# Performance work log

Hardware: AMD Instinct MI355X
Metric: run time of the kernel (lower is better)

Reference implementation:

```python
import jax, jax.numpy as jnp
import numpy as np

D_MODEL = 512
D_FFN = 2048
N_LAYERS = 6
VOCAB = 1000
D_STATE = 16
D_CONV = 4
D_INNER = 2 * D_MODEL  # expand=2
DT_RANK = 32           # ceil(d_model/16)
B, LT, LS = 2, 512, 512


def _pos_encoding(length, d_model):
    pos = np.arange(length, dtype=np.float32)[:, None]
    div = np.exp(np.arange(0, d_model, 2, dtype=np.float32) * (-np.log(10000.0) / d_model))
    pe = np.zeros((length, d_model), np.float32)
    pe[:, 0::2] = np.sin(pos * div)
    pe[:, 1::2] = np.cos(pos * div)
    return jnp.asarray(pe)


def _layer_norm(x, g, b, eps=1e-6):
    m = x.mean(-1, keepdims=True)
    v = ((x - m) ** 2).mean(-1, keepdims=True)
    return (x - m) * jax.lax.rsqrt(v + eps) * g + b


def _mamba(x, in_w, conv_w, conv_b, xproj_w, dt_w, dt_b, A_log, Dskip, out_w):
    # x: (b, l, d_model)
    b, l, _ = x.shape
    xz = x @ in_w.T                                   # (b, l, 2*d_inner)
    xc, z = jnp.split(xz, 2, axis=-1)
    # causal depthwise conv over time
    xt = jnp.transpose(xc, (0, 2, 1))                 # (b, d_inner, l)
    xt = jnp.pad(xt, ((0, 0), (0, 0), (D_CONV - 1, 0)))
    xt = jax.lax.conv_general_dilated(
        xt, conv_w, window_strides=(1,), padding='VALID',
        feature_group_count=D_INNER, dimension_numbers=('NCH', 'OIH', 'NCH'))
    xc = jax.nn.silu(jnp.transpose(xt, (0, 2, 1)) + conv_b)  # (b, l, d_inner)
    dbl = xc @ xproj_w.T                              # (b, l, dt_rank + 2*n)
    dt, Bm, Cm = jnp.split(dbl, [DT_RANK, DT_RANK + D_STATE], axis=-1)
    dt = jax.nn.softplus(dt @ dt_w.T + dt_b)          # (b, l, d_inner)
    A = -jnp.exp(A_log)                               # (d_inner, n)

    def step(h, xs):
        dt_t, B_t, C_t, u_t = xs                      # (b,d),(b,n),(b,n),(b,d)
        dA = jnp.exp(dt_t[..., None] * A)             # (b, d, n)
        h = dA * h + (dt_t * u_t)[..., None] * B_t[:, None, :]
        y = jnp.einsum('bdn,bn->bd', h, C_t)
        return h, y

    h0 = jnp.zeros((b, D_INNER, D_STATE), x.dtype)
    xs = (jnp.swapaxes(dt, 0, 1), jnp.swapaxes(Bm, 0, 1),
          jnp.swapaxes(Cm, 0, 1), jnp.swapaxes(xc, 0, 1))
    _, ys = jax.lax.scan(step, h0, xs)                # ys: (l, b, d_inner)
    y = jnp.swapaxes(ys, 0, 1) + xc * Dskip
    y = y * jax.nn.silu(z)
    return y @ out_w.T                                # (b, l, d_model)


def setup_inputs() -> dict:
    key = jax.random.key(0)
    ks = iter(jax.random.split(key, 40))

    def rn(shape, s=0.02):
        return jax.random.normal(next(ks), shape, jnp.float32) * s

    def mamba_params():
        return dict(
            in_w=rn((N_LAYERS, 2 * D_INNER, D_MODEL)),
            conv_w=rn((N_LAYERS, D_INNER, 1, D_CONV), 0.1),
            conv_b=rn((N_LAYERS, D_INNER)),
            xproj=rn((N_LAYERS, DT_RANK + 2 * D_STATE, D_INNER)),
            dtw=rn((N_LAYERS, D_INNER, DT_RANK)),
            dtb=rn((N_LAYERS, D_INNER)),
            Alog=jnp.log(jnp.broadcast_to(jnp.arange(1.0, D_STATE + 1.0, dtype=jnp.float32), (N_LAYERS, D_INNER, D_STATE))),
            D=jnp.ones((N_LAYERS, D_INNER), jnp.float32),
            outw=rn((N_LAYERS, D_MODEL, D_INNER)),
        )

    ps, pc = mamba_params(), mamba_params()
    inp = {
        'src': jax.random.normal(next(ks), (B, LS, D_MODEL), jnp.float32),
        'tgt': jax.random.randint(next(ks), (B, LT), 0, VOCAB),
        'emb': rn((VOCAB, D_MODEL)),
        'in_w_s': ps['in_w'], 'conv_w_s': ps['conv_w'], 'conv_b_s': ps['conv_b'],
        'xproj_s': ps['xproj'], 'dtw_s': ps['dtw'], 'dtb_s': ps['dtb'],
        'Alog_s': ps['Alog'], 'D_s': ps['D'], 'outw_s': ps['outw'],
        'in_w_c': pc['in_w'], 'conv_w_c': pc['conv_w'], 'conv_b_c': pc['conv_b'],
        'xproj_c': pc['xproj'], 'dtw_c': pc['dtw'], 'dtb_c': pc['dtb'],
        'Alog_c': pc['Alog'], 'D_c': pc['D'], 'outw_c': pc['outw'],
        'ffn_w1': rn((N_LAYERS, D_FFN, D_MODEL)),
        'ffn_b1': jnp.zeros((N_LAYERS, D_FFN), jnp.float32),
        'ffn_w2': rn((N_LAYERS, D_MODEL, D_FFN)),
        'ffn_b2': jnp.zeros((N_LAYERS, D_MODEL), jnp.float32),
        'ln_g': jnp.ones((N_LAYERS, 3, D_MODEL), jnp.float32),
        'ln_b': jnp.zeros((N_LAYERS, 3, D_MODEL), jnp.float32),
        'fin_g': jnp.ones((D_MODEL,), jnp.float32),
        'fin_b': jnp.zeros((D_MODEL,), jnp.float32),
    }
    return inp


def reference(src, tgt, emb, in_w_s, conv_w_s, conv_b_s, xproj_s, dtw_s, dtb_s,
              Alog_s, D_s, outw_s, in_w_c, conv_w_c, conv_b_c, xproj_c, dtw_c,
              dtb_c, Alog_c, D_c, outw_c, ffn_w1, ffn_b1, ffn_w2, ffn_b2,
              ln_g, ln_b, fin_g, fin_b):
    # NormalizedEmbedding + sinusoidal positional encoding
    x = emb[tgt] * jnp.sqrt(jnp.asarray(D_MODEL, jnp.float32))
    x = x + _pos_encoding(LT, D_MODEL)[None]
    for i in range(N_LAYERS):
        # self mamba (post-norm, normalize_before=False)
        t2 = _mamba(x, in_w_s[i], conv_w_s[i], conv_b_s[i], xproj_s[i],
                    dtw_s[i], dtb_s[i], Alog_s[i], D_s[i], outw_s[i])
        x = _layer_norm(x + t2, ln_g[i, 0], ln_b[i, 0])
        # cross mamba over concat([memory, tgt]) then take last LT steps
        cat = jnp.concatenate([src, x], axis=1)
        t2 = _mamba(cat, in_w_c[i], conv_w_c[i], conv_b_c[i], xproj_c[i],
                    dtw_c[i], dtb_c[i], Alog_c[i], D_c[i], outw_c[i])[:, -LT:]
        x = _layer_norm(x + t2, ln_g[i, 1], ln_b[i, 1])
        # positionwise FFN
        h = jax.nn.relu(x @ ffn_w1[i].T + ffn_b1[i]) @ ffn_w2[i].T + ffn_b2[i]
        x = _layer_norm(x + h, ln_g[i, 2], ln_b[i, 2])
    return _layer_norm(x, fin_g, fin_b)
```

## Files before the change

kernel.cpp:

```cpp
#include <hip/hip_runtime.h>
#include <math.h>

#define DMODEL 512
#define DINNER 1024
#define DSTATE 16
#define DTRANK 32
#define NLAYERS 6
#define BB 2
#define LT 512
#define LS 512

typedef __attribute__((ext_vector_type(8))) short bf16x8;
typedef __attribute__((ext_vector_type(8))) unsigned short u16x8;
typedef __attribute__((ext_vector_type(4))) float f32x4;

__device__ __forceinline__ unsigned short f2bf(float f) {
  unsigned u = __float_as_uint(f);
  u += 0x7fffu + ((u >> 16) & 1u);
  return (unsigned short)(u >> 16);
}
__device__ __forceinline__ float bf2f(unsigned short u) {
  return __uint_as_float((unsigned)u << 16);
}

template<int EPI>
__device__ __forceinline__ float epi_apply(float acc, float b) {
  if (EPI == 1) { float v = acc + b; return v > 0.f ? v : 0.f; }
  if (EPI == 2) { return acc + b; }
  if (EPI == 3) { float v = acc + b; return fmaxf(v, 0.f) + log1pf(__expf(-fabsf(v))); }
  return acc;
}

__global__ __launch_bounds__(256) void cvt_all_kernel(
    const float* __restrict__ i0, const float* __restrict__ i1,
    const float* __restrict__ i2, const float* __restrict__ i3,
    const float* __restrict__ i4, const float* __restrict__ i5,
    const float* __restrict__ i6, const float* __restrict__ i7,
    const float* __restrict__ i8, const float* __restrict__ i9,
    unsigned short* __restrict__ outbase) {
  int i = blockIdx.x * 256 + threadIdx.x;
  if (i >= 8159232) return;
  const float* in; int off;
  if      (i < 1572864) { in = i0; off = i; }
  else if (i < 3145728) { in = i1; off = i - 1572864; }
  else if (i < 3244032) { in = i2; off = i - 3145728; }
  else if (i < 3342336) { in = i3; off = i - 3244032; }
  else if (i < 3391488) { in = i4; off = i - 3342336; }
  else if (i < 3440640) { in = i5; off = i - 3391488; }
  else if (i < 4227072) { in = i6; off = i - 3440640; }
  else if (i < 5013504) { in = i7; off = i - 4227072; }
  else if (i < 6586368) { in = i8; off = i - 5013504; }
  else                  { in = i9; off = i - 6586368; }
  float4 a = ((const float4*)in)[off];
  ushort4 o = make_ushort4(f2bf(a.x), f2bf(a.y), f2bf(a.z), f2bf(a.w));
  *(ushort4*)&outbase[(size_t)i * 4] = o;
}

__global__ __launch_bounds__(256) void embed_kernel(const int* __restrict__ tgt,
    const float* __restrict__ emb, float* __restrict__ X,
    unsigned short* __restrict__ Xb) {
  int i = blockIdx.x * 256 + threadIdx.x;
  int d = i & (DMODEL - 1);
  int bt = i >> 9;
  int t = bt & (LT - 1);
  int tok = tgt[bt];
  float div = __expf((float)(d & ~1) * (-9.210340371976184f / (float)DMODEL));
  float ang = (float)t * div;
  float pe = (d & 1) ? cosf(ang) : sinf(ang);
  float v = emb[(size_t)tok * DMODEL + d] * 22.627416997969522f + pe;
  X[i] = v;
  Xb[i] = f2bf(v);
}

__global__ __launch_bounds__(256) void catsrc_kernel(const float* __restrict__ src,
    unsigned short* __restrict__ CATb) {
  int i = blockIdx.x * 256 + threadIdx.x;
  int c8 = (i & 63) * 8;
  int r = i >> 6;
  int b = r >> 9, l = r & 511;
  const float* s = src + ((size_t)b * 512 + l) * DMODEL + c8;
  float4 a = *(const float4*)s;
  float4 bq = *(const float4*)(s + 4);
  u16x8 o;
  o[0] = f2bf(a.x); o[1] = f2bf(a.y); o[2] = f2bf(a.z); o[3] = f2bf(a.w);
  o[4] = f2bf(bq.x); o[5] = f2bf(bq.y); o[6] = f2bf(bq.z); o[7] = f2bf(bq.w);
  *(u16x8*)&CATb[((size_t)b * 1024 + l) * DMODEL + c8] = o;
}

template<int BK, int EPI, bool SPLIT, bool OUTB>
__global__ __launch_bounds__(256) void mgemmA(
    const unsigned short* __restrict__ A, const unsigned short* __restrict__ Bw,
    const float* __restrict__ bias, float* __restrict__ C,
    unsigned short* __restrict__ Cb, int M, int N, int K, int lda) {
  constexpr int PAD = BK + 8;
  constexpr int CHA = BK / 32;
  constexpr int CHB = BK / 16;
  __shared__ __align__(16) unsigned short As[64 * PAD];
  __shared__ __align__(16) unsigned short Bs[128 * PAD];
  const int tid = threadIdx.x;
  const int bn = blockIdx.x * 128;
  const int bm = blockIdx.y * 64;
  const int lane = tid & 63;
  const int w = tid >> 6;
  const int wr = (w >> 1) * 32;
  const int wc = (w & 1) * 64;
  const int l15 = lane & 15;
  const int l4 = lane >> 4;
  const int koff = l4 * 8;
  int kcnt = K, kbeg = 0;
  if (SPLIT) { kcnt = K / (int)gridDim.z; kbeg = blockIdx.z * kcnt; }
  const int nt = kcnt / BK;
  f32x4 acc[2][4] = {};

  int arow_[CHA], ak8_[CHA];
  const unsigned short* Ap[CHA];
#pragma unroll
  for (int i = 0; i < CHA; ++i) {
    int f = tid + 256 * i;
    arow_[i] = f / (BK / 8);
    ak8_[i] = (f % (BK / 8)) * 8;
    Ap[i] = A + (size_t)(bm + arow_[i]) * lda + kbeg + ak8_[i];
  }
  int brow_[CHB], bk8_[CHB];
  const unsigned short* Bp[CHB];
#pragma unroll
  for (int i = 0; i < CHB; ++i) {
    int f = tid + 256 * i;
    brow_[i] = f / (BK / 8);
    bk8_[i] = (f % (BK / 8)) * 8;
    Bp[i] = Bw + (size_t)(bn + brow_[i]) * K + kbeg + bk8_[i];
  }

  u16x8 av[CHA], bv[CHB];
#pragma unroll
  for (int i = 0; i < CHA; ++i) av[i] = *(const u16x8*)Ap[i];
#pragma unroll
  for (int i = 0; i < CHB; ++i) bv[i] = *(const u16x8*)Bp[i];

  for (int t = 0; t < nt; ++t) {
    __syncthreads();
#pragma unroll
    for (int i = 0; i < CHA; ++i) *(u16x8*)&As[arow_[i] * PAD + ak8_[i]] = av[i];
#pragma unroll
    for (int i = 0; i < CHB; ++i) *(u16x8*)&Bs[brow_[i] * PAD + bk8_[i]] = bv[i];
    if (t + 1 < nt) {
      int ko = (t + 1) * BK;
#pragma unroll
      for (int i = 0; i < CHA; ++i) av[i] = *(const u16x8*)(Ap[i] + ko);
#pragma unroll
      for (int i = 0; i < CHB; ++i) bv[i] = *(const u16x8*)(Bp[i] + ko);
    }
    __syncthreads();
#pragma unroll
    for (int kk = 0; kk < BK / 32; ++kk) {
      bf16x8 afr[2], bfr[4];
#pragma unroll
      for (int i = 0; i < 2; ++i)
        afr[i] = *(const bf16x8*)&As[(wr + i * 16 + l15) * PAD + kk * 32 + koff];
#pragma unroll
      for (int j = 0; j < 4; ++j)
        bfr[j] = *(const bf16x8*)&Bs[(wc + j * 16 + l15) * PAD + kk * 32 + koff];
#pragma unroll
      for (int fr = 0; fr < 2; ++fr)
#pragma unroll
        for (int fc = 0; fc < 4; ++fc)
          acc[fr][fc] = __builtin_amdgcn_mfma_f32_16x16x32_bf16(
              afr[fr], bfr[fc], acc[fr][fc], 0, 0, 0);
    }
  }

  if (SPLIT) {
    float* Pz = C + (size_t)blockIdx.z * M * N;
#pragma unroll
    for (int fc = 0; fc < 4; ++fc) {
      int col = bn + wc + fc * 16 + l15;
#pragma unroll
      for (int fr = 0; fr < 2; ++fr) {
        int row0 = bm + wr + fr * 16 + l4 * 4;
#pragma unroll
        for (int r = 0; r < 4; ++r)
          Pz[(size_t)(row0 + r) * N + col] = acc[fr][fc][r];
      }
    }
  } else {
#pragma unroll
    for (int fc = 0; fc < 4; ++fc) {
      int col = bn + wc + fc * 16 + l15;
      float bvs = (EPI != 0) ? bias[col] : 0.f;
#pragma unroll
      for (int fr = 0; fr < 2; ++fr) {
        int row0 = bm + wr + fr * 16 + l4 * 4;
#pragma unroll
        for (int r = 0; r < 4; ++r) {
          float v = epi_apply<EPI>(acc[fr][fc][r], bvs);
          if (OUTB) Cb[(size_t)(row0 + r) * N + col] = f2bf(v);
          else      C[(size_t)(row0 + r) * N + col] = v;
        }
      }
    }
  }
}

template<int BK, int EPI, bool SPLIT, bool OUTB>
__global__ __launch_bounds__(256) void mgemm(
    const unsigned short* __restrict__ A, const unsigned short* __restrict__ Bw,
    const float* __restrict__ bias, float* __restrict__ C,
    unsigned short* __restrict__ Cb, int M, int N, int K, int lda) {
  constexpr int PAD = BK + 8;
  constexpr int CH = BK / 32;
  __shared__ __align__(16) unsigned short As[64 * PAD];
  __shared__ __align__(16) unsigned short Bs[64 * PAD];
  const int tid = threadIdx.x;
  const int bn = blockIdx.x * 64;
  const int bm = blockIdx.y * 64;
  const int lane = tid & 63;
  const int w = tid >> 6;
  const int wr = (w >> 1) * 32;
  const int wc = (w & 1) * 32;
  const int l15 = lane & 15;
  const int l4 = lane >> 4;
  const int koff = l4 * 8;
  int kcnt = K, kbeg = 0;
  if (SPLIT) { kcnt = K / (int)gridDim.z; kbeg = blockIdx.z * kcnt; }
  const int nt = kcnt / BK;
  f32x4 acc[2][2] = {};

  int row_[CH], k8_[CH];
  const unsigned short *Ap[CH], *Bp[CH];
#pragma unroll
  for (int i = 0; i < CH; ++i) {
    int f = tid + 256 * i;
    row_[i] = f / (BK / 8);
    k8_[i] = (f % (BK / 8)) * 8;
    Ap[i] = A + (size_t)(bm + row_[i]) * lda + kbeg + k8_[i];
    Bp[i] = Bw + (size_t)(bn + row_[i]) * K + kbeg + k8_[i];
  }

  u16x8 av[CH], bv[CH];
#pragma unroll
  for (int i = 0; i < CH; ++i) { av[i] = *(const u16x8*)Ap[i]; bv[i] = *(const u16x8*)Bp[i]; }

  for (int t = 0; t < nt; ++t) {
    __syncthreads();
#pragma unroll
    for (int i = 0; i < CH; ++i) {
      *(u16x8*)&As[row_[i] * PAD + k8_[i]] = av[i];
      *(u16x8*)&Bs[row_[i] * PAD + k8_[i]] = bv[i];
    }
    if (t + 1 < nt) {
      int ko = (t + 1) * BK;
#pragma unroll
      for (int i = 0; i < CH; ++i) {
        av[i] = *(const u16x8*)(Ap[i] + ko);
        bv[i] = *(const u16x8*)(Bp[i] + ko);
      }
    }
    __syncthreads();
#pragma unroll
    for (int kk = 0; kk < CH; ++kk) {
      bf16x8 afr[2], bfr[2];
#pragma unroll
      for (int i = 0; i < 2; ++i) {
        afr[i] = *(const bf16x8*)&As[(wr + i * 16 + l15) * PAD + kk * 32 + koff];
        bfr[i] = *(const bf16x8*)&Bs[(wc + i * 16 + l15) * PAD + kk * 32 + koff];
      }
#pragma unroll
      for (int fr = 0; fr < 2; ++fr)
#pragma unroll
        for (int fc = 0; fc < 2; ++fc)
          acc[fr][fc] = __builtin_amdgcn_mfma_f32_16x16x32_bf16(
              afr[fr], bfr[fc], acc[fr][fc], 0, 0, 0);
    }
  }

  if (SPLIT) {
    float* Pz = C + (size_t)blockIdx.z * M * N;
#pragma unroll
    for (int fc = 0; fc < 2; ++fc) {
      int col = bn + wc + fc * 16 + l15;
#pragma unroll
      for (int fr = 0; fr < 2; ++fr) {
        int row0 = bm + wr + fr * 16 + l4 * 4;
#pragma unroll
        for (int r = 0; r < 4; ++r)
          Pz[(size_t)(row0 + r) * N + col] = acc[fr][fc][r];
      }
    }
  } else {
#pragma unroll
    for (int fc = 0; fc < 2; ++fc) {
      int col = bn + wc + fc * 16 + l15;
      float bvs = (EPI != 0) ? bias[col] : 0.f;
#pragma unroll
      for (int fr = 0; fr < 2; ++fr) {
        int row0 = bm + wr + fr * 16 + l4 * 4;
#pragma unroll
        for (int r = 0; r < 4; ++r) {
          float v = epi_apply<EPI>(acc[fr][fc][r], bvs);
          if (OUTB) Cb[(size_t)(row0 + r) * N + col] = f2bf(v);
          else      C[(size_t)(row0 + r) * N + col] = v;
        }
      }
    }
  }
}

__global__ __launch_bounds__(256) void mgemm_dt(
    const float* __restrict__ XPP, const unsigned short* __restrict__ Bw,
    const float* __restrict__ bias, unsigned short* __restrict__ Cb,
    int M, int N) {
  constexpr int PAD = 40;
  __shared__ __align__(16) unsigned short As[64 * PAD];
  __shared__ __align__(16) unsigned short Bs[64 * PAD];
  const int tid = threadIdx.x;
  const int bn = blockIdx.x * 64;
  const int bm = blockIdx.y * 64;
  const int lane = tid & 63;
  const int w = tid >> 6;
  const int wr = (w >> 1) * 32;
  const int wc = (w & 1) * 32;
  const int l15 = lane & 15;
  const int l4 = lane >> 4;
  const int koff = l4 * 8;
  const size_t zs = (size_t)M * 64;
  {
    int r = tid >> 2, c8 = (tid & 3) * 8;
    const float* p = XPP + (size_t)(bm + r) * 64 + c8;
    float s[8] = {0.f, 0.f, 0.f, 0.f, 0.f, 0.f, 0.f, 0.f};
#pragma unroll
    for (int z = 0; z < 8; ++z) {
      float4 a = *(const float4*)(p + z * zs);
      float4 b = *(const float4*)(p + z * zs + 4);
      s[0] += a.x; s[1] += a.y; s[2] += a.z; s[3] += a.w;
      s[4] += b.x; s[5] += b.y; s[6] += b.z; s[7] += b.w;
    }
    u16x8 o;
#pragma unroll
    for (int j = 0; j < 8; ++j) o[j] = f2bf(s[j]);
    *(u16x8*)&As[r * PAD + c8] = o;
    *(u16x8*)&Bs[r * PAD + c8] = *(const u16x8*)(Bw + (size_t)(bn + r) * 32 + c8);
  }
  __syncthreads();
  bf16x8 afr[2], bfr[2];
#pragma unroll
  for (int i = 0; i < 2; ++i) {
    afr[i] = *(const bf16x8*)&As[(wr + i * 16 + l15) * PAD + koff];
    bfr[i] = *(const bf16x8*)&Bs[(wc + i * 16 + l15) * PAD + koff];
  }
  f32x4 acc[2][2] = {};
#pragma unroll
  for (int fr = 0; fr < 2; ++fr)
#pragma unroll
    for (int fc = 0; fc < 2; ++fc)
      acc[fr][fc] = __builtin_amdgcn_mfma_f32_16x16x32_bf16(
          afr[fr], bfr[fc], acc[fr][fc], 0, 0, 0);
#pragma unroll
  for (int fc = 0; fc < 2; ++fc) {
    int col = bn + wc + fc * 16 + l15;
    float bvs = bias[col];
#pragma unroll
    for (int fr = 0; fr < 2; ++fr) {
      int row0 = bm + wr + fr * 16 + l4 * 4;
#pragma unroll
      for (int r = 0; r < 4; ++r)
        Cb[(size_t)(row0 + r) * N + col] = f2bf(epi_apply<3>(acc[fr][fc][r], bvs));
    }
  }
}

__global__ __launch_bounds__(256) void conv_silu_kernel(
    const unsigned short* __restrict__ xzb, const float* __restrict__ w,
    const float* __restrict__ bias, unsigned short* __restrict__ outb, int L) {
  int idx = blockIdx.x * 256 + threadIdx.x;
  int d8 = (idx & 127) * 8;
  int bt = idx >> 7;
  int b = bt / L;
  int t = bt - b * L;
  const unsigned short* col = xzb + ((size_t)b * L) * (2 * DINNER) + d8;
  float acc[8];
  float4 wv[8];
#pragma unroll
  for (int j = 0; j < 8; ++j) {
    acc[j] = bias[d8 + j];
    wv[j] = *(const float4*)(w + (size_t)(d8 + j) * 4);
  }
#pragma unroll
  for (int k = 0; k < 4; ++k) {
    int tt = t - 3 + k;
    if (tt >= 0) {
      u16x8 v = *(const u16x8*)(col + (size_t)tt * (2 * DINNER));
      float wk[8] = {
        k == 0 ? wv[0].x : k == 1 ? wv[0].y : k == 2 ? wv[0].z : wv[0].w,
        k == 0 ? wv[1].x : k == 1 ? wv[1].y : k == 2 ? wv[1].z : wv[1].w,
        k == 0 ? wv[2].x : k == 1 ? wv[2].y : k == 2 ? wv[2].z : wv[2].w,
        k == 0 ? wv[3].x : k == 1 ? wv[3].y : k == 2 ? wv[3].z : wv[3].w,
        k == 0 ? wv[4].x : k == 1 ? wv[4].y : k == 2 ? wv[4].z : wv[4].w,
        k == 0 ? wv[5].x : k == 1 ? wv[5].y : k == 2 ? wv[5].z : wv[5].w,
        k == 0 ? wv[6].x : k == 1 ? wv[6].y : k == 2 ? wv[6].z : wv[6].w,
        k == 0 ? wv[7].x : k == 1 ? wv[7].y : k == 2 ? wv[7].z : wv[7].w };
#pragma unroll
      for (int j = 0; j < 8; ++j) acc[j] = fmaf(bf2f(v[j]), wk[j], acc[j]);
    }
  }
  u16x8 o;
#pragma unroll
  for (int j = 0; j < 8; ++j) {
    float sig = 1.f / (1.f + __expf(-acc[j]));
    o[j] = f2bf(acc[j] * sig);
  }
  *(u16x8*)&outb[(size_t)bt * DINNER + d8] = o;
}

__global__ __launch_bounds__(256) void scan_pass1(
    const unsigned short* __restrict__ dt, const float* __restrict__ XPP,
    const unsigned short* __restrict__ u, const float* __restrict__ Alog,
    float* __restrict__ P, float* __restrict__ S, int L, int CL) {
  __shared__ float BC[32][32];
  const int tid = threadIdx.x;
  const int d = blockIdx.x * 256 + tid;
  const int b = blockIdx.y;
  const int c = blockIdx.z;
  const int t0 = c * CL;
  if (tid < CL * 4) {
    int t = tid >> 2, j8 = (tid & 3) * 8;
    const float* p = XPP + ((size_t)b * L + t0 + t) * 64 + 32 + j8;
    const size_t zs = (size_t)BB * L * 64;
    float s[8] = {0.f, 0.f, 0.f, 0.f, 0.f, 0.f, 0.f, 0.f};
#pragma unroll
    for (int z = 0; z < 8; ++z) {
      float4 a = *(const float4*)(p + z * zs);
      float4 bq = *(const float4*)(p + z * zs + 4);
      s[0] += a.x; s[1] += a.y; s[2] += a.z; s[3] += a.w;
      s[4] += bq.x; s[5] += bq.y; s[6] += bq.z; s[7] += bq.w;
    }
#pragma unroll
    for (int j = 0; j < 8; ++j) BC[t][j8 + j] = s[j];
  }
  float A[16], h[16], Pp[16];
#pragma unroll
  for (int j = 0; j < 4; ++j) {
    float4 a4 = *(const float4*)(Alog + d * 16 + j * 4);
    A[j * 4 + 0] = -__expf(a4.x); A[j * 4 + 1] = -__expf(a4.y);
    A[j * 4 + 2] = -__expf(a4.z); A[j * 4 + 3] = -__expf(a4.w);
  }
#pragma unroll
  for (int n = 0; n < 16; ++n) { h[n] = 0.f; Pp[n] = 1.f; }
  const unsigned short* dtp = dt + ((size_t)b * L + t0) * DINNER + d;
  const unsigned short* up  = u  + ((size_t)b * L + t0) * DINNER + d;
  __syncthreads();
  float dtv = bf2f(dtp[0]), uv = bf2f(up[0]);
  for (int t = 0; t < CL; ++t) {
    float dtn = 0.f, un = 0.f;
    if (t + 1 < CL) {
      dtn = bf2f(dtp[(size_t)(t + 1) * DINNER]);
      un  = bf2f(up[(size_t)(t + 1) * DINNER]);
    }
    float du = dtv * uv;
#pragma unroll
    for (int n = 0; n < 16; ++n) {
      float dA = __expf(dtv * A[n]);
      Pp[n] *= dA;
      h[n] = fmaf(dA, h[n], du * BC[t][n]);
    }
    dtv = dtn; uv = un;
  }
  size_t base = (size_t)c * 32768 + ((size_t)(b * 1024 + d) << 4);
#pragma unroll
  for (int j = 0; j < 4; ++j) {
    *(float4*)&P[base + j * 4] = make_float4(Pp[j*4], Pp[j*4+1], Pp[j*4+2], Pp[j*4+3]);
    *(float4*)&S[base + j * 4] = make_float4(h[j*4], h[j*4+1], h[j*4+2], h[j*4+3]);
  }
}

__global__ __launch_bounds__(256) void scan_pass2(
    const unsigned short* __restrict__ dt, const float* __restrict__ XPP,
    const unsigned short* __restrict__ u, const unsigned short* __restrict__ xzb,
    const float* __restrict__ Alog, const float* __restrict__ Dsk,
    const float* __restrict__ P, const float* __restrict__ S,
    unsigned short* __restrict__ ysb, int L, int CL, int c0) {
  __shared__ float BC[32][32];
  const int tid = threadIdx.x;
  const int d = blockIdx.x * 256 + tid;
  const int b = blockIdx.y;
  const int c = blockIdx.z + c0;
  const int t0 = c * CL;
  if (tid < CL * 4) {
    int t = tid >> 2, j8 = (tid & 3) * 8;
    const float* p = XPP + ((size_t)b * L + t0 + t) * 64 + 32 + j8;
    const size_t zs = (size_t)BB * L * 64;
    float s[8] = {0.f, 0.f, 0.f, 0.f, 0.f, 0.f, 0.f, 0.f};
#pragma unroll
    for (int z = 0; z < 8; ++z) {
      float4 a = *(const float4*)(p + z * zs);
      float4 bq = *(const float4*)(p + z * zs + 4);
      s[0] += a.x; s[1] += a.y; s[2] += a.z; s[3] += a.w;
      s[4] += bq.x; s[5] += bq.y; s[6] += bq.z; s[7] += bq.w;
    }
#pragma unroll
    for (int j = 0; j < 8; ++j) BC[t][j8 + j] = s[j];
  }
  float A[16], h[16];
#pragma unroll
  for (int j = 0; j < 4; ++j) {
    float4 a4 = *(const float4*)(Alog + d * 16 + j * 4);
    A[j * 4 + 0] = -__expf(a4.x); A[j * 4 + 1] = -__expf(a4.y);
    A[j * 4 + 2] = -__expf(a4.z); A[j * 4 + 3] = -__expf(a4.w);
  }
#pragma unroll
  for (int n = 0; n < 16; ++n) h[n] = 0.f;
  size_t sbase = (size_t)(b * 1024 + d) << 4;
  for (int cc = 0; cc < c; ++cc) {
    size_t bb = (size_t)cc * 32768 + sbase;
#pragma unroll
    for (int j = 0; j < 4; ++j) {
      float4 p4 = *(const float4*)&P[bb + j * 4];
      float4 s4 = *(const float4*)&S[bb + j * 4];
      h[j*4+0] = fmaf(p4.x, h[j*4+0], s4.x);
      h[j*4+1] = fmaf(p4.y, h[j*4+1], s4.y);
      h[j*4+2] = fmaf(p4.z, h[j*4+2], s4.z);
      h[j*4+3] = fmaf(p4.w, h[j*4+3], s4.w);
    }
  }
  float Dv = Dsk[d];
  const unsigned short* dtp = dt + ((size_t)b * L + t0) * DINNER + d;
  const unsigned short* up  = u  + ((size_t)b * L + t0) * DINNER + d;
  const unsigned short* zp  = xzb + ((size_t)b * L + t0) * (2 * DINNER) + DINNER + d;
  unsigned short* yp = ysb + ((size_t)(b * 512) + (t0 - c0 * CL)) * DINNER + d;
  __syncthreads();
  float dtv = bf2f(dtp[0]), uv = bf2f(up[0]), zv = bf2f(zp[0]);
  for (int t = 0; t < CL; ++t) {
    float dtn = 0.f, un = 0.f, zn = 0.f;
    if (t + 1 < CL) {
      dtn = bf2f(dtp[(size_t)(t + 1) * DINNER]);
      un  = bf2f(up[(size_t)(t + 1) * DINNER]);
      zn  = bf2f(zp[(size_t)(t + 1) * (2 * DINNER)]);
    }
    float du = dtv * uv;
    float y = 0.f;
#pragma unroll
    for (int n = 0; n < 16; ++n) {
      float dA = __expf(dtv * A[n]);
      h[n] = fmaf(dA, h[n], du * BC[t][n]);
      y = fmaf(h[n], BC[t][16 + n], y);
    }
    float sig = 1.f / (1.f + __expf(-zv));
    yp[(size_t)t * DINNER] = f2bf((y + uv * Dv) * (zv * sig));
    dtv = dtn; uv = un; zv = zn;
  }
}

template<int NZ, int EPI>
__global__ __launch_bounds__(64) void ln_red_kernel(
    const float* __restrict__ res, const float* __restrict__ P,
    const float* __restrict__ bias, const float* __restrict__ g,
    const float* __restrict__ be, float* __restrict__ out,
    unsigned short* __restrict__ outb, int row_scale, int row_off) {
  int r = blockIdx.x;
  int b = r >> 9, t = r & 511;
  int lane = threadIdx.x;
  const float* rp = res + (size_t)r * DMODEL;
  size_t ob = ((size_t)(b * row_scale + row_off + t)) * DMODEL;
  float v[8];
  float s = 0.f, ss = 0.f;
#pragma unroll
  for (int j = 0; j < 8; ++j) {
    int col = lane + j * 64;
    float acc = 0.f;
#pragma unroll
    for (int z = 0; z < NZ; ++z) acc += P[(size_t)z * 524288 + (size_t)r * DMODEL + col];
    float bv = (EPI != 0) ? bias[col] : 0.f;
    float x = rp[col] + epi_apply<EPI>(acc, bv);
    v[j] = x; s += x; ss += x * x;
  }
#pragma unroll
  for (int o = 32; o > 0; o >>= 1) { s += __shfl_xor(s, o); ss += __shfl_xor(ss, o); }
  float m = s * (1.f / 512.f);
  float var = ss * (1.f / 512.f) - m * m;
  float rs = rsqrtf(var + 1e-6f);
#pragma unroll
  for (int j = 0; j < 8; ++j) {
    int col = lane + j * 64;
    float o2 = (v[j] - m) * rs * g[col] + be[col];
    out[(size_t)r * DMODEL + col] = o2;
    outb[ob + col] = f2bf(o2);
  }
}

__global__ __launch_bounds__(64) void ln_final_kernel(
    const float* __restrict__ res, const float* __restrict__ g,
    const float* __restrict__ be, float* __restrict__ out) {
  int r = blockIdx.x;
  int lane = threadIdx.x;
  const float* rp = res + (size_t)r * DMODEL;
  float v[8];
  float s = 0.f, ss = 0.f;
#pragma unroll
  for (int j = 0; j < 8; ++j) {
    float x = rp[lane + j * 64];
    v[j] = x; s += x; ss += x * x;
  }
#pragma unroll
  for (int o = 32; o > 0; o >>= 1) { s += __shfl_xor(s, o); ss += __shfl_xor(ss, o); }
  float m = s * (1.f / 512.f);
  float var = ss * (1.f / 512.f) - m * m;
  float rs = rsqrtf(var + 1e-6f);
#pragma unroll
  for (int j = 0; j < 8; ++j) {
    int c = lane + j * 64;
    out[(size_t)r * DMODEL + c] = (v[j] - m) * rs * g[c] + be[c];
  }
}

extern "C" void kernel_launch(void* const* d_in, const int* in_sizes, int n_in,
                              void* d_out, int out_size, void* d_ws, size_t ws_size,
                              hipStream_t stream) {
  (void)in_sizes; (void)n_in; (void)out_size; (void)ws_size;
  const float* src      = (const float*)d_in[0];
  const int*   tgt      = (const int*)d_in[1];
  const float* emb      = (const float*)d_in[2];
  const float* in_w_s   = (const float*)d_in[3];
  const float* conv_w_s = (const float*)d_in[4];
  const float* conv_b_s = (const float*)d_in[5];
  const float* xproj_s  = (const float*)d_in[6];
  const float* dtw_s    = (const float*)d_in[7];
  const float* dtb_s    = (const float*)d_in[8];
  const float* Alog_s   = (const float*)d_in[9];
  const float* D_s      = (const float*)d_in[10];
  const float* outw_s   = (const float*)d_in[11];
  const float* in_w_c   = (const float*)d_in[12];
  const float* conv_w_c = (const float*)d_in[13];
  const float* conv_b_c = (const float*)d_in[14];
  const float* xproj_c  = (const float*)d_in[15];
  const float* dtw_c    = (const float*)d_in[16];
  const float* dtb_c    = (const float*)d_in[17];
  const float* Alog_c   = (const float*)d_in[18];
  const float* D_c      = (const float*)d_in[19];
  const float* outw_c   = (const float*)d_in[20];
  const float* ffn_w1   = (const float*)d_in[21];
  const float* ffn_b1   = (const float*)d_in[22];
  const float* ffn_w2   = (const float*)d_in[23];
  const float* ffn_b2   = (const float*)d_in[24];
  const float* ln_g     = (const float*)d_in[25];
  const float* ln_b     = (const float*)d_in[26];
  const float* fin_g    = (const float*)d_in[27];
  const float* fin_b    = (const float*)d_in[28];

  float* ws   = (float*)d_ws;
  float* X    = ws;
  float* XZ   = X + 524288;
  float* XPP  = XZ + 4194304;
  float* SC_P = XPP + 1048576;
  float* SC_S = SC_P + 1048576;
  unsigned short* U = (unsigned short*)(SC_S + 1048576);
  unsigned short* Xb   = U;
  unsigned short* CATb = Xb + 524288;
  unsigned short* XCb  = CATb + 1048576;
  unsigned short* XZb  = XCb + 2097152;
  unsigned short* YSb  = XZb + 4194304;
  unsigned short* DTb  = YSb + 1048576;
  unsigned short* WB   = DTb + 2097152;
  unsigned short* inwsb = WB;
  unsigned short* inwcb = inwsb + 6291456;
  unsigned short* xpsb  = inwcb + 6291456;
  unsigned short* xpcb  = xpsb + 393216;
  unsigned short* dtwsb = xpcb + 393216;
  unsigned short* dtwcb = dtwsb + 196608;
  unsigned short* owsb  = dtwcb + 196608;
  unsigned short* owcb  = owsb + 3145728;
  unsigned short* f1b   = owcb + 3145728;
  unsigned short* f2b   = f1b + 6291456;

  cvt_all_kernel<<<31872, 256, 0, stream>>>(
      in_w_s, in_w_c, xproj_s, xproj_c, dtw_s, dtw_c, outw_s, outw_c,
      ffn_w1, ffn_w2, WB);
  embed_kernel<<<2048, 256, 0, stream>>>(tgt, emb, X, Xb);
  catsrc_kernel<<<256, 256, 0, stream>>>(src, CATb);

  for (int i = 0; i < NLAYERS; ++i) {
    mgemmA<64, 0, false, true><<<dim3(16, 16), 256, 0, stream>>>(
        Xb, inwsb + (size_t)i * 1048576, nullptr, nullptr, XZb, 1024, 2048, 512, 512);
    conv_silu_kernel<<<512, 256, 0, stream>>>(
        XZb, conv_w_s + (size_t)i * 4096, conv_b_s + (size_t)i * 1024, XCb, 512);
    mgemm<64, 0, true, false><<<dim3(1, 16, 8), 256, 0, stream>>>(
        XCb, xpsb + (size_t)i * 65536, nullptr, XPP, nullptr, 1024, 64, 1024, 1024);
    mgemm_dt<<<dim3(16, 16), 256, 0, stream>>>(
        XPP, dtwsb + (size_t)i * 32768, dtb_s + (size_t)i * 1024, DTb, 1024, 1024);
    scan_pass1<<<dim3(4, 2, 32), 256, 0, stream>>>(
        DTb, XPP, XCb, Alog_s + (size_t)i * 16384, SC_P, SC_S, 512, 16);
    scan_pass2<<<dim3(4, 2, 32), 256, 0, stream>>>(
        DTb, XPP, XCb, XZb, Alog_s + (size_t)i * 16384, D_s + (size_t)i * 1024,
        SC_P, SC_S, YSb, 512, 16, 0);
    mgemmA<64, 0, true, false><<<dim3(4, 16, 4), 256, 0, stream>>>(
        YSb, owsb + (size_t)i * 524288, nullptr, XZ, nullptr, 1024, 512, 1024, 1024);
    ln_red_kernel<4, 0><<<1024, 64, 0, stream>>>(
        X, XZ, nullptr, ln_g + (size_t)(i * 3 + 0) * 512,
        ln_b + (size_t)(i * 3 + 0) * 512, X, CATb, 1024, 512);

    mgemmA<64, 0, false, true><<<dim3(16, 32), 256, 0, stream>>>(
        CATb, inwcb + (size_t)i * 1048576, nullptr, nullptr, XZb, 2048, 2048, 512, 512);
    conv_silu_kernel<<<1024, 256, 0, stream>>>(
        XZb, conv_w_c + (size_t)i * 4096, conv_b_c + (size_t)i * 1024, XCb, 1024);
    mgemm<64, 0, true, false><<<dim3(1, 32, 8), 256, 0, stream>>>(
        XCb, xpcb + (size_t)i * 65536, nullptr, XPP, nullptr, 2048, 64, 1024, 1024);
    mgemm_dt<<<dim3(16, 32), 256, 0, stream>>>(
        XPP, dtwcb + (size_t)i * 32768, dtb_c + (size_t)i * 1024, DTb, 2048, 1024);
    scan_pass1<<<dim3(4, 2, 32), 256, 0, stream>>>(
        DTb, XPP, XCb, Alog_c + (size_t)i * 16384, SC_P, SC_S, 1024, 32);
    scan_pass2<<<dim3(4, 2, 16), 256, 0, stream>>>(
        DTb, XPP, XCb, XZb, Alog_c + (size_t)i * 16384, D_c + (size_t)i * 1024,
        SC_P, SC_S, YSb, 1024, 32, 16);
    mgemmA<64, 0, true, false><<<dim3(4, 16, 4), 256, 0, stream>>>(
        YSb, owcb + (size_t)i * 524288, nullptr, XZ, nullptr, 1024, 512, 1024, 1024);
    ln_red_kernel<4, 0><<<1024, 64, 0, stream>>>(
        X, XZ, nullptr, ln_g + (size_t)(i * 3 + 1) * 512,
        ln_b + (size_t)(i * 3 + 1) * 512, X, Xb, 512, 0);

    mgemmA<64, 1, false, true><<<dim3(16, 16), 256, 0, stream>>>(
        Xb, f1b + (size_t)i * 1048576, ffn_b1 + (size_t)i * 2048, nullptr, XZb,
        1024, 2048, 512, 512);
    mgemmA<64, 0, true, false><<<dim3(4, 16, 8), 256, 0, stream>>>(
        XZb, f2b + (size_t)i * 1048576, nullptr, XZ, nullptr, 1024, 512, 2048, 2048);
    ln_red_kernel<8, 2><<<1024, 64, 0, stream>>>(
        X, XZ, ffn_b2 + (size_t)i * 512, ln_g + (size_t)(i * 3 + 2) * 512,
        ln_b + (size_t)(i * 3 + 2) * 512, X, Xb, 512, 0);
  }

  ln_final_kernel<<<1024, 64, 0, stream>>>(X, fin_g, fin_b, (float*)d_out);
}
```

Measured before the change: 1.194 ms.

## Fuse fp32-to-bf16 weight conversion into GEMM tile loads, drop upfront cvt pass

Removes the separate kernel that converted every fp32 weight tensor to bf16 before the layer loop. The GEMM kernels now read fp32 weights directly and round them to bf16 while staging tiles into shared memory. This saves one full pass over the weights, but each GEMM now reads twice the weight bytes and does extra conversion ALU work, and weights reused across M-tiles are converted repeatedly. Some launches also change tile kernel and grid choices: the in-projection and FFN1 GEMMs switch to the smaller 64x64 kernel, and the out-projection uses more split-K slices.

```diff
diff --git a/kernel.cpp b/kernel.cpp
--- a/kernel.cpp
+++ b/kernel.cpp
@@ -29,31 +29,6 @@
   if (EPI == 2) { return acc + b; }
   if (EPI == 3) { float v = acc + b; return fmaxf(v, 0.f) + log1pf(__expf(-fabsf(v))); }
   return acc;
-}
-
-__global__ __launch_bounds__(256) void cvt_all_kernel(
-    const float* __restrict__ i0, const float* __restrict__ i1,
-    const float* __restrict__ i2, const float* __restrict__ i3,
-    const float* __restrict__ i4, const float* __restrict__ i5,
-    const float* __restrict__ i6, const float* __restrict__ i7,
-    const float* __restrict__ i8, const float* __restrict__ i9,
-    unsigned short* __restrict__ outbase) {
-  int i = blockIdx.x * 256 + threadIdx.x;
-  if (i >= 8159232) return;
-  const float* in; int off;
-  if      (i < 1572864) { in = i0; off = i; }
-  else if (i < 3145728) { in = i1; off = i - 1572864; }
-  else if (i < 3244032) { in = i2; off = i - 3145728; }
-  else if (i < 3342336) { in = i3; off = i - 3244032; }
-  else if (i < 3391488) { in = i4; off = i - 3342336; }
-  else if (i < 3440640) { in = i5; off = i - 3391488; }
-  else if (i < 4227072) { in = i6; off = i - 3440640; }
-  else if (i < 5013504) { in = i7; off = i - 4227072; }
-  else if (i < 6586368) { in = i8; off = i - 5013504; }
-  else                  { in = i9; off = i - 6586368; }
-  float4 a = ((const float4*)in)[off];
-  ushort4 o = make_ushort4(f2bf(a.x), f2bf(a.y), f2bf(a.z), f2bf(a.w));
-  *(ushort4*)&outbase[(size_t)i * 4] = o;
 }
 
 __global__ __launch_bounds__(256) void embed_kernel(const int* __restrict__ tgt,
@@ -89,7 +64,7 @@
 
 template<int BK, int EPI, bool SPLIT, bool OUTB>
 __global__ __launch_bounds__(256) void mgemmA(
-    const unsigned short* __restrict__ A, const unsigned short* __restrict__ Bw,
+    const unsigned short* __restrict__ A, const float* __restrict__ Bw,
     const float* __restrict__ bias, float* __restrict__ C,
     unsigned short* __restrict__ Cb, int M, int N, int K, int lda) {
   constexpr int PAD = BK + 8;
@@ -122,7 +97,7 @@
     Ap[i] = A + (size_t)(bm + arow_[i]) * lda + kbeg + ak8_[i];
   }
   int brow_[CHB], bk8_[CHB];
-  const unsigned short* Bp[CHB];
+  const float* Bp[CHB];
 #pragma unroll
   for (int i = 0; i < CHB; ++i) {
     int f = tid + 256 * i;
@@ -131,24 +106,36 @@
     Bp[i] = Bw + (size_t)(bn + brow_[i]) * K + kbeg + bk8_[i];
   }
 
-  u16x8 av[CHA], bv[CHB];
+  u16x8 av[CHA];
+  float4 bv0[CHB], bv1[CHB];
 #pragma unroll
   for (int i = 0; i < CHA; ++i) av[i] = *(const u16x8*)Ap[i];
 #pragma unroll
-  for (int i = 0; i < CHB; ++i) bv[i] = *(const u16x8*)Bp[i];
+  for (int i = 0; i < CHB; ++i) {
+    bv0[i] = *(const float4*)Bp[i];
+    bv1[i] = *(const float4*)(Bp[i] + 4);
+  }
 
   for (int t = 0; t < nt; ++t) {
     __syncthreads();
 #pragma unroll
     for (int i = 0; i < CHA; ++i) *(u16x8*)&As[arow_[i] * PAD + ak8_[i]] = av[i];
 #pragma unroll
-    for (int i = 0; i < CHB; ++i) *(u16x8*)&Bs[brow_[i] * PAD + bk8_[i]] = bv[i];
+    for (int i = 0; i < CHB; ++i) {
+      u16x8 o;
+      o[0] = f2bf(bv0[i].x); o[1] = f2bf(bv0[i].y); o[2] = f2bf(bv0[i].z); o[3] = f2bf(bv0[i].w);
+      o[4] = f2bf(bv1[i].x); o[5] = f2bf(bv1[i].y); o[6] = f2bf(bv1[i].z); o[7] = f2bf(bv1[i].w);
+      *(u16x8*)&Bs[brow_[i] * PAD + bk8_[i]] = o;
+    }
     if (t + 1 < nt) {
       int ko = (t + 1) * BK;
 #pragma unroll
       for (int i = 0; i < CHA; ++i) av[i] = *(const u16x8*)(Ap[i] + ko);
 #pragma unroll
-      for (int i = 0; i < CHB; ++i) bv[i] = *(const u16x8*)(Bp[i] + ko);
+      for (int i = 0; i < CHB; ++i) {
+        bv0[i] = *(const float4*)(Bp[i] + ko);
+        bv1[i] = *(const float4*)(Bp[i] + ko + 4);
+      }
     }
     __syncthreads();
 #pragma unroll
@@ -203,7 +190,7 @@
 
 template<int BK, int EPI, bool SPLIT, bool OUTB>
 __global__ __launch_bounds__(256) void mgemm(
-    const unsigned short* __restrict__ A, const unsigned short* __restrict__ Bw,
+    const unsigned short* __restrict__ A, const float* __restrict__ Bw,
     const float* __restrict__ bias, float* __restrict__ C,
     unsigned short* __restrict__ Cb, int M, int N, int K, int lda) {
   constexpr int PAD = BK + 8;
@@ -226,7 +213,8 @@
   f32x4 acc[2][2] = {};
 
   int row_[CH], k8_[CH];
-  const unsigned short *Ap[CH], *Bp[CH];
+  const unsigned short* Ap[CH];
+  const float* Bp[CH];
 #pragma unroll
   for (int i = 0; i < CH; ++i) {
     int f = tid + 256 * i;
@@ -236,23 +224,32 @@
     Bp[i] = Bw + (size_t)(bn + row_[i]) * K + kbeg + k8_[i];
   }
 
-  u16x8 av[CH], bv[CH];
-#pragma unroll
-  for (int i = 0; i < CH; ++i) { av[i] = *(const u16x8*)Ap[i]; bv[i] = *(const u16x8*)Bp[i]; }
+  u16x8 av[CH];
+  float4 bv0[CH], bv1[CH];
+#pragma unroll
+  for (int i = 0; i < CH; ++i) {
+    av[i] = *(const u16x8*)Ap[i];
+    bv0[i] = *(const float4*)Bp[i];
+    bv1[i] = *(const float4*)(Bp[i] + 4);
+  }
 
   for (int t = 0; t < nt; ++t) {
     __syncthreads();
 #pragma unroll
     for (int i = 0; i < CH; ++i) {
       *(u16x8*)&As[row_[i] * PAD + k8_[i]] = av[i];
-      *(u16x8*)&Bs[row_[i] * PAD + k8_[i]] = bv[i];
+      u16x8 o;
+      o[0] = f2bf(bv0[i].x); o[1] = f2bf(bv0[i].y); o[2] = f2bf(bv0[i].z); o[3] = f2bf(bv0[i].w);
+      o[4] = f2bf(bv1[i].x); o[5] = f2bf(bv1[i].y); o[6] = f2bf(bv1[i].z); o[7] = f2bf(bv1[i].w);
+      *(u16x8*)&Bs[row_[i] * PAD + k8_[i]] = o;
     }
     if (t + 1 < nt) {
       int ko = (t + 1) * BK;
 #pragma unroll
       for (int i = 0; i < CH; ++i) {
         av[i] = *(const u16x8*)(Ap[i] + ko);
-        bv[i] = *(const u16x8*)(Bp[i] + ko);
+        bv0[i] = *(const float4*)(Bp[i] + ko);
+        bv1[i] = *(const float4*)(Bp[i] + ko + 4);
       }
     }
     __syncthreads();
@@ -306,7 +303,7 @@
 }
 
 __global__ __launch_bounds__(256) void mgemm_dt(
-    const float* __restrict__ XPP, const unsigned short* __restrict__ Bw,
+    const float* __restrict__ XPP, const float* __restrict__ Bw,
     const float* __restrict__ bias, unsigned short* __restrict__ Cb,
     int M, int N) {
   constexpr int PAD = 40;
@@ -338,7 +335,13 @@
 #pragma unroll
     for (int j = 0; j < 8; ++j) o[j] = f2bf(s[j]);
     *(u16x8*)&As[r * PAD + c8] = o;
-    *(u16x8*)&Bs[r * PAD + c8] = *(const u16x8*)(Bw + (size_t)(bn + r) * 32 + c8);
+    const float* bw = Bw + (size_t)(bn + r) * 32 + c8;
+    float4 b0 = *(const float4*)bw;
+    float4 b1 = *(const float4*)(bw + 4);
+    u16x8 ob;
+    ob[0] = f2bf(b0.x); ob[1] = f2bf(b0.y); ob[2] = f2bf(b0.z); ob[3] = f2bf(b0.w);
+    ob[4] = f2bf(b1.x); ob[5] = f2bf(b1.y); ob[6] = f2bf(b1.z); ob[7] = f2bf(b1.w);
+    *(u16x8*)&Bs[r * PAD + c8] = ob;
   }
   __syncthreads();
   bf16x8 afr[2], bfr[2];
@@ -658,68 +661,54 @@
   unsigned short* XZb  = XCb + 2097152;
   unsigned short* YSb  = XZb + 4194304;
   unsigned short* DTb  = YSb + 1048576;
-  unsigned short* WB   = DTb + 2097152;
-  unsigned short* inwsb = WB;
-  unsigned short* inwcb = inwsb + 6291456;
-  unsigned short* xpsb  = inwcb + 6291456;
-  unsigned short* xpcb  = xpsb + 393216;
-  unsigned short* dtwsb = xpcb + 393216;
-  unsigned short* dtwcb = dtwsb + 196608;
-  unsigned short* owsb  = dtwcb + 196608;
-  unsigned short* owcb  = owsb + 3145728;
-  unsigned short* f1b   = owcb + 3145728;
-  unsigned short* f2b   = f1b + 6291456;
-
-  cvt_all_kernel<<<31872, 256, 0, stream>>>(
-      in_w_s, in_w_c, xproj_s, xproj_c, dtw_s, dtw_c, outw_s, outw_c,
-      ffn_w1, ffn_w2, WB);
+
   embed_kernel<<<2048, 256, 0, stream>>>(tgt, emb, X, Xb);
   catsrc_kernel<<<256, 256, 0, stream>>>(src, CATb);
 
   for (int i = 0; i < NLAYERS; ++i) {
-    mgemmA<64, 0, false, true><<<dim3(16, 16), 256, 0, stream>>>(
-        Xb, inwsb + (size_t)i * 1048576, nullptr, nullptr, XZb, 1024, 2048, 512, 512);
+    mgemm<64, 0, false, true><<<dim3(32, 16), 256, 0, stream>>>(
+        Xb, in_w_s + (size_t)i * 1048576, nullptr, nullptr, XZb, 1024, 2048, 512, 512);
     conv_silu_kernel<<<512, 256, 0, stream>>>(
         XZb, conv_w_s + (size_t)i * 4096, conv_b_s + (size_t)i * 1024, XCb, 512);
     mgemm<64, 0, true, false><<<dim3(1, 16, 8), 256, 0, stream>>>(
-        XCb, xpsb + (size_t)i * 65536, nullptr, XPP, nullptr, 1024, 64, 1024, 1024);
+        XCb, xproj_s + (size_t)i * 65536, nullptr, XPP, nullptr, 1024, 64, 1024, 1024);
     mgemm_dt<<<dim3(16, 16), 256, 0, stream>>>(
-        XPP, dtwsb + (size_t)i * 32768, dtb_s + (size_t)i * 1024, DTb, 1024, 1024);
+        XPP, dtw_s + (size_t)i * 32768, dtb_s + (size_t)i * 1024, DTb, 1024, 1024);
     scan_pass1<<<dim3(4, 2, 32), 256, 0, stream>>>(
         DTb, XPP, XCb, Alog_s + (size_t)i * 16384, SC_P, SC_S, 512, 16);
     scan_pass2<<<dim3(4, 2, 32), 256, 0, stream>>>(
         DTb, XPP, XCb, XZb, Alog_s + (size_t)i * 16384, D_s + (size_t)i * 1024,
         SC_P, SC_S, YSb, 512, 16, 0);
-    mgemmA<64, 0, true, false><<<dim3(4, 16, 4), 256, 0, stream>>>(
-        YSb, owsb + (size_t)i * 524288, nullptr, XZ, nullptr, 1024, 512, 1024, 1024);
-    ln_red_kernel<4, 0><<<1024, 64, 0, stream>>>(
+    mgemmA<64, 0, true, false><<<dim3(4, 16, 8), 256, 0, stream>>>(
+        YSb, outw_s + (size_t)i * 524288, nullptr, XZ, nullptr, 1024, 512, 1024, 1024);
+    ln_red_kernel<8, 0><<<1024, 64, 0, stream>>>(
         X, XZ, nullptr, ln_g + (size_t)(i * 3 + 0) * 512,
         ln_b + (size_t)(i * 3 + 0) * 512, X, CATb, 1024, 512);
 
     mgemmA<64, 0, false, true><<<dim3(16, 32), 256, 0, stream>>>(
-        CATb, inwcb + (size_t)i * 1048576, nullptr, nullptr, XZb, 2048, 2048, 512, 512);
+        CATb, in_w_c + (size_t)i * 1048576, nullptr, nullptr, XZb, 2048, 2048, 512, 512);
     conv_silu_kernel<<<1024, 256, 0, stream>>>(
         XZb, conv_w_c + (size_t)i * 4096, conv_b_c + (size_t)i * 1024, XCb, 1024);
     mgemm<64, 0, true, false><<<dim3(1, 32, 8), 256, 0, stream>>>(
-        XCb, xpcb + (size_t)i * 65536, nullptr, XPP, nullptr, 2048, 64, 1024, 1024);
+        XCb, xproj_c + (size_t)i * 65536, nullptr, XPP, nullptr, 2048, 64, 1024, 1024);
     mgemm_dt<<<dim3(16, 32), 256, 0, stream>>>(
-        XPP, dtwcb + (size_t)i * 32768, dtb_c + (size_t)i * 1024, DTb, 2048, 1024);
+        XPP, dtw_c + (size_t)i * 32768, dtb_c + (size_t)i * 1024, DTb, 2048, 1024);
     scan_pass1<<<dim3(4, 2, 32), 256, 0, stream>>>(
         DTb, XPP, XCb, Alog_c + (size_t)i * 16384, SC_P, SC_S, 1024, 32);
     scan_pass2<<<dim3(4, 2, 16), 256, 0, stream>>>(
         DTb, XPP, XCb, XZb, Alog_c + (size_t)i * 16384, D_c + (size_t)i * 1024,
         SC_P, SC_S, YSb, 1024, 32, 16);
-    mgemmA<64, 0, true, false><<<dim3(4, 16, 4), 256, 0, stream>>>(
-        YSb, owcb + (size_t)i * 524288, nullptr, XZ, nullptr, 1024, 512, 1024, 1024);
-    ln_red_kernel<4, 0><<<1024, 64, 0, stream>>>(
+    mgemmA<64, 0, true, false><<<dim3(4, 16, 8), 256, 0, stream>>>(
+        YSb, outw_c + (size_t)i * 524288, nullptr, XZ, nullptr, 1024, 512, 1024, 1024);
+    ln_red_kernel<8, 0><<<1024, 64, 0, stream>>>(
         X, XZ, nullptr, ln_g + (size_t)(i * 3 + 1) * 512,
         ln_b + (size_t)(i * 3 + 1) * 512, X, Xb, 512, 0);
 
-    mgemmA<64, 1, false, true><<<dim3(16, 16), 256, 0, stream>>>(
-        Xb, f1b + (size_t)i * 1048576, ffn_b1 + (size_t)i * 2048, nullptr, XZb,
+    mgemm<64, 1, false, true><<<dim3(32, 16), 256, 0, stream>>>(
+        Xb, ffn_w1 + (size_t)i * 1048576, ffn_b1 + (size_t)i * 2048, nullptr, XZb,
         1024, 2048, 512, 512);
     mgemmA<64, 0, true, false><<<dim3(4, 16, 8), 256, 0, stream>>>(
-        XZb, f2b + (size_t)i * 1048576, nullptr, XZ, nullptr, 1024, 512, 2048, 2048);
+        XZb, ffn_w2 + (size_t)i * 1048576, nullptr, XZ, nullptr, 1024, 512, 2048, 2048);
     ln_red_kernel<8, 2><<<1024, 64, 0, stream>>>(
         X, XZ, ffn_b2 + (size_t)i * 512, ln_g + (size_t)(i * 3 + 2) * 512,
         ln_b + (size_t)(i * 3 + 2) * 512, X, Xb, 512, 0);
```

Result: slower. 1.243 ms (+4.1%).
